# Kernel optimization log

Hardware: AMD Instinct MI355X
Metric: run time of the kernel (lower is better)

Reference implementation:

```python
import jax, jax.numpy as jnp
import numpy as np

B, D, S = 256, 8192, 8      # batch, conv dim (2*d_model), new tokens per request
W = 4                        # conv kernel width
NSLOTS = 2048                # cache slots
STATE_LEN = W - 1


def setup_inputs() -> dict:
    key = jax.random.key(0)
    k1, k2, k3, k4 = jax.random.split(key, 4)
    x = jax.random.normal(k1, (B, D, S), dtype=jnp.float32)
    weight = jax.random.normal(k2, (D, W), dtype=jnp.float32) * 0.1
    conv_states = jax.random.normal(k3, (NSLOTS, D, STATE_LEN), dtype=jnp.float32)
    # unique slot per request to avoid scatter collisions (matches paged-cache usage)
    cache_indices = jax.random.permutation(k4, NSLOTS)[:B].astype(jnp.int64)
    return {"x": x, "weight": weight, "conv_states": conv_states,
            "cache_indices": cache_indices, "residual_connection": 1,
            "pad_slot_id": -1}


def reference(x, weight, conv_states, cache_indices, residual_connection, pad_slot_id):
    # x: [B, D, S]; weight: [D, W]; conv_states: [NSLOTS, D, W-1]
    b, d, s = x.shape
    w = weight.shape[1]
    state_len = conv_states.shape[-1]
    valid = cache_indices != pad_slot_id                      # [B]
    safe_idx = jnp.where(valid, cache_indices, 0)
    st = conv_states[safe_idx]                                # gather: [B, D, state_len]
    cat = jnp.concatenate([st, x], axis=-1)                   # [B, D, state_len + S]
    # causal depthwise conv: out[..., t] = sum_k cat[..., t+k] * weight[:, k]
    windows = jnp.stack([cat[..., k:k + s] for k in range(w)], axis=-1)  # [B, D, S, W]
    out = jnp.einsum('bdsw,dw->bds', windows, weight)
    if residual_connection:
        out = out + x                                          # fused residual add
    # masked rows (pad_slot_id) produce output but do not update the cache
    new_state = cat[..., -state_len:]                          # [B, D, state_len]
    upd = jnp.where(valid[:, None, None], new_state, st)
    new_conv_states = conv_states.at[safe_idx].set(upd)        # scatter back
    return out, new_conv_states
```

## Files before the change

kernel.cpp:

```cpp
#include <hip/hip_runtime.h>

#define BB 256
#define DD 8192
#define SS 8
#define NSLOTS 2048
#define STATE_LEN 3

#define CONV_BLOCKS (BB * (DD / 256))
#define COPY_CHUNKS 6
#define COPY_BLOCKS (NSLOTS * COPY_CHUNKS)

typedef float f4 __attribute__((ext_vector_type(4)));

__global__ __launch_bounds__(256)
void build_flags(const int* __restrict__ cache_indices,
                 const int* __restrict__ pad_p,
                 int* __restrict__ flag) {
    const int t = threadIdx.x;
#pragma unroll
    for (int k = 0; k < NSLOTS / 256; ++k) flag[t + k * 256] = 0;
    __syncthreads();
    const int ci = cache_indices[t];
    if (ci != pad_p[0] && ci >= 0 && ci < NSLOTS) flag[ci] = 1;
}

__global__ __launch_bounds__(256)
void fused_conv_state_kernel(const float* __restrict__ x,
                             const float* __restrict__ weight,
                             const float* __restrict__ conv_states,
                             const int* __restrict__ cache_indices,
                             const int* __restrict__ residual_p,
                             const int* __restrict__ pad_p,
                             const int* __restrict__ flag,
                             float* __restrict__ out,
                             float* __restrict__ out_ns) {
    const int bid = blockIdx.x;
    const int tid = threadIdx.x;

    if (bid >= CONV_BLOCKS) {
        const int cid = bid - CONV_BLOCKS;
        const int n   = cid / COPY_CHUNKS;
        const int c   = cid - n * COPY_CHUNKS;
        if (flag[n]) return;
        const size_t base4 = (size_t)n * (DD * STATE_LEN / 4)
                           + (size_t)c * 1024 + tid;
        const f4* __restrict__ src = (const f4*)conv_states;
        f4* __restrict__ dst = (f4*)out_ns;
#pragma unroll
        for (int k = 0; k < 4; ++k) {
            f4 v = __builtin_nontemporal_load(src + base4 + k * 256);
            __builtin_nontemporal_store(v, dst + base4 + k * 256);
        }
        return;
    }

    const int b      = bid >> 5;
    const int dchunk = bid & 31;
    const int d      = (dchunk << 8) | tid;

    const int  ci    = cache_indices[b];
    const bool valid = (ci != pad_p[0]);
    const int  slot  = valid ? ci : 0;

    const size_t sbase = ((size_t)slot * DD + d) * STATE_LEN;
    const float s0 = conv_states[sbase];
    const float s1 = conv_states[sbase + 1];
    const float s2 = conv_states[sbase + 2];

    const f4* __restrict__ xr = (const f4*)(x + ((size_t)b * DD + d) * SS);
    const f4 x0 = xr[0];
    const f4 x1 = xr[1];
    const f4 wv = ((const f4*)weight)[d];

    const float cat[11] = {s0, s1, s2,
                           x0.x, x0.y, x0.z, x0.w,
                           x1.x, x1.y, x1.z, x1.w};
    float o[8];
#pragma unroll
    for (int s = 0; s < SS; ++s) {
        o[s] = cat[s] * wv.x + cat[s + 1] * wv.y +
               cat[s + 2] * wv.z + cat[s + 3] * wv.w;
    }
    if (residual_p[0]) {
        o[0] += x0.x; o[1] += x0.y; o[2] += x0.z; o[3] += x0.w;
        o[4] += x1.x; o[5] += x1.y; o[6] += x1.z; o[7] += x1.w;
    }

    f4* __restrict__ orow = (f4*)(out + ((size_t)b * DD + d) * SS);
    orow[0] = (f4){o[0], o[1], o[2], o[3]};
    orow[1] = (f4){o[4], o[5], o[6], o[7]};

    if (valid) {
        out_ns[sbase]     = x1.y;
        out_ns[sbase + 1] = x1.z;
        out_ns[sbase + 2] = x1.w;
    }
}

extern "C" void kernel_launch(void* const* d_in, const int* in_sizes, int n_in,
                              void* d_out, int out_size, void* d_ws, size_t ws_size,
                              hipStream_t stream) {
    const float* x           = (const float*)d_in[0];
    const float* weight      = (const float*)d_in[1];
    const float* conv_states = (const float*)d_in[2];
    const int*   cache_idx   = (const int*)d_in[3];
    const int*   residual_p  = (const int*)d_in[4];
    const int*   pad_p       = (const int*)d_in[5];

    float* out    = (float*)d_out;
    float* out_ns = out + (size_t)BB * DD * SS;
    int*   flag   = (int*)d_ws;

    build_flags<<<1, 256, 0, stream>>>(cache_idx, pad_p, flag);
    fused_conv_state_kernel<<<CONV_BLOCKS + COPY_BLOCKS, 256, 0, stream>>>(
        x, weight, conv_states, cache_idx, residual_p, pad_p, flag, out, out_ns);
}
```

Before: 435.7 us.

## Drop flag-building kernel, check slot membership per copy block, widen copy chunks

Removes the separate build_flags launch. Each copy block now decides whether its slot is overwritten by scanning cache_indices with a wavefront vote. Copy blocks now move 8 vectors per thread instead of 4, with all loads issued before the stores, which halves the number of copy blocks. The conv path switches its loads and stores to nontemporal to avoid polluting the cache. The trade-off is redundant index scanning in every copy block and possible cache effects from the nontemporal hints.

```diff
diff --git a/kernel.cpp b/kernel.cpp
--- a/kernel.cpp
+++ b/kernel.cpp
@@ -7,22 +7,10 @@
 #define STATE_LEN 3
 
 #define CONV_BLOCKS (BB * (DD / 256))
-#define COPY_CHUNKS 6
+#define COPY_CHUNKS 3
 #define COPY_BLOCKS (NSLOTS * COPY_CHUNKS)
 
 typedef float f4 __attribute__((ext_vector_type(4)));
-
-__global__ __launch_bounds__(256)
-void build_flags(const int* __restrict__ cache_indices,
-                 const int* __restrict__ pad_p,
-                 int* __restrict__ flag) {
-    const int t = threadIdx.x;
-#pragma unroll
-    for (int k = 0; k < NSLOTS / 256; ++k) flag[t + k * 256] = 0;
-    __syncthreads();
-    const int ci = cache_indices[t];
-    if (ci != pad_p[0] && ci >= 0 && ci < NSLOTS) flag[ci] = 1;
-}
 
 __global__ __launch_bounds__(256)
 void fused_conv_state_kernel(const float* __restrict__ x,
@@ -31,7 +19,6 @@
                              const int* __restrict__ cache_indices,
                              const int* __restrict__ residual_p,
                              const int* __restrict__ pad_p,
-                             const int* __restrict__ flag,
                              float* __restrict__ out,
                              float* __restrict__ out_ns) {
     const int bid = blockIdx.x;
@@ -41,16 +28,29 @@
         const int cid = bid - CONV_BLOCKS;
         const int n   = cid / COPY_CHUNKS;
         const int c   = cid - n * COPY_CHUNKS;
-        if (flag[n]) return;
+
+        {
+            const int lane = tid & 63;
+            const int4 ci4 = ((const int4*)cache_indices)[lane];
+            const int pad = pad_p[0];
+            const bool m = (ci4.x == n && ci4.x != pad) ||
+                           (ci4.y == n && ci4.y != pad) ||
+                           (ci4.z == n && ci4.z != pad) ||
+                           (ci4.w == n && ci4.w != pad);
+            if (__any(m)) return;
+        }
+
         const size_t base4 = (size_t)n * (DD * STATE_LEN / 4)
-                           + (size_t)c * 1024 + tid;
+                           + (size_t)c * 2048 + tid;
         const f4* __restrict__ src = (const f4*)conv_states;
         f4* __restrict__ dst = (f4*)out_ns;
+        f4 v[8];
 #pragma unroll
-        for (int k = 0; k < 4; ++k) {
-            f4 v = __builtin_nontemporal_load(src + base4 + k * 256);
-            __builtin_nontemporal_store(v, dst + base4 + k * 256);
-        }
+        for (int k = 0; k < 8; ++k)
+            v[k] = __builtin_nontemporal_load(src + base4 + k * 256);
+#pragma unroll
+        for (int k = 0; k < 8; ++k)
+            __builtin_nontemporal_store(v[k], dst + base4 + k * 256);
         return;
     }
 
@@ -63,13 +63,13 @@
     const int  slot  = valid ? ci : 0;
 
     const size_t sbase = ((size_t)slot * DD + d) * STATE_LEN;
-    const float s0 = conv_states[sbase];
-    const float s1 = conv_states[sbase + 1];
-    const float s2 = conv_states[sbase + 2];
+    const float s0 = __builtin_nontemporal_load(conv_states + sbase);
+    const float s1 = __builtin_nontemporal_load(conv_states + sbase + 1);
+    const float s2 = __builtin_nontemporal_load(conv_states + sbase + 2);
 
     const f4* __restrict__ xr = (const f4*)(x + ((size_t)b * DD + d) * SS);
-    const f4 x0 = xr[0];
-    const f4 x1 = xr[1];
+    const f4 x0 = __builtin_nontemporal_load(xr);
+    const f4 x1 = __builtin_nontemporal_load(xr + 1);
     const f4 wv = ((const f4*)weight)[d];
 
     const float cat[11] = {s0, s1, s2,
@@ -87,13 +87,13 @@
     }
 
     f4* __restrict__ orow = (f4*)(out + ((size_t)b * DD + d) * SS);
-    orow[0] = (f4){o[0], o[1], o[2], o[3]};
-    orow[1] = (f4){o[4], o[5], o[6], o[7]};
+    __builtin_nontemporal_store((f4){o[0], o[1], o[2], o[3]}, orow);
+    __builtin_nontemporal_store((f4){o[4], o[5], o[6], o[7]}, orow + 1);
 
     if (valid) {
-        out_ns[sbase]     = x1.y;
-        out_ns[sbase + 1] = x1.z;
-        out_ns[sbase + 2] = x1.w;
+        __builtin_nontemporal_store(x1.y, out_ns + sbase);
+        __builtin_nontemporal_store(x1.z, out_ns + sbase + 1);
+        __builtin_nontemporal_store(x1.w, out_ns + sbase + 2);
     }
 }
 
@@ -109,9 +109,7 @@
 
     float* out    = (float*)d_out;
     float* out_ns = out + (size_t)BB * DD * SS;
-    int*   flag   = (int*)d_ws;
 
-    build_flags<<<1, 256, 0, stream>>>(cache_idx, pad_p, flag);
     fused_conv_state_kernel<<<CONV_BLOCKS + COPY_BLOCKS, 256, 0, stream>>>(
-        x, weight, conv_states, cache_idx, residual_p, pad_p, flag, out, out_ns);
+        x, weight, conv_states, cache_idx, residual_p, pad_p, out, out_ns);
 }
```

After: 437.7 us. No clear change (+0.5%).
